# Kernel tuning notes

Measured on AMD Instinct MI355X. Metric: run time of the kernel, lower is better.

The kernel has to match this reference:

```python
import jax, jax.numpy as jnp
import numpy as np

CAPACITY_FACTOR = 1.2


def setup_inputs() -> dict:
    key = jax.random.key(0)
    k1, k2 = jax.random.split(key, 2)
    D, E = 1024, 64
    x = jax.random.normal(k1, (8, 4096, D), dtype=jnp.float32)
    # xavier-uniform-ish router weight, zero bias (as in __init__)
    limit = np.sqrt(6.0 / (D + E)).astype(np.float32)
    W = jax.random.uniform(k2, (E, D), dtype=jnp.float32, minval=-limit, maxval=limit)
    b = jnp.zeros((E,), dtype=jnp.float32)
    return {"x": x, "W": W, "b": b, "detach_inputs": 0}


def reference(x, W, b, detach_inputs):
    bsz, seqlen, D = x.shape
    E = W.shape[0]                      # num experts == max_steps
    N = bsz * seqlen                    # num tokens
    x_flat = x.reshape(N, D)
    if detach_inputs:
        x_flat = jax.lax.stop_gradient(x_flat)
    logits = x_flat @ W.T + b           # [N, E]

    # expert-choice capacity (static python ints)
    k = max(1, int(N / max(1, E) * CAPACITY_FACTOR))
    k = min(k, N)

    # per-expert top-k over tokens: [E, k]
    topk_vals, topk_idx = jax.lax.top_k(logits.T, k)
    cand_tok = topk_idx.reshape(-1)                       # [E*k] token ids
    cand_exp = jnp.repeat(jnp.arange(E, dtype=jnp.int32), k)  # [E*k]
    cand_val = topk_vals.reshape(-1)                      # [E*k]

    # scatter-amax: best candidate logit per token (torch scatter_reduce_ 'amax')
    best_val = jnp.full((N,), -jnp.inf, dtype=logits.dtype).at[cand_tok].max(cand_val)

    # candidates that achieve the per-token max; dedup -> one expert per token
    # (tie-break: smallest expert index, matching first-occurrence after sort)
    eq = cand_val == best_val[cand_tok]
    exp_cand = jnp.where(eq, cand_exp, E).astype(jnp.int32)
    token_exp = jnp.full((N,), E, dtype=jnp.int32).at[cand_tok].min(exp_cand)
    selected = token_exp < E                              # token was picked by some expert
    assigned_expert = jnp.where(selected, token_exp, -1)  # [N], -1 = unassigned

    # load-balance loss from per-expert counts (bincount of assigned experts)
    sel_f = selected.astype(logits.dtype)
    counts = jnp.zeros((E,), dtype=logits.dtype).at[jnp.where(selected, token_exp, 0)].add(sel_f)
    mean_load = counts.mean()
    load_balance_loss = ((counts - mean_load) ** 2).mean() / (mean_load + 1e-9)

    best_val_out = jnp.where(selected, best_val, jnp.zeros((), logits.dtype))
    return (best_val_out, assigned_expert, selected, load_balance_loss)
```

## Files before the change

### kernel.cpp

```cpp
#include <hip/hip_runtime.h>
#include <math.h>

typedef __attribute__((ext_vector_type(4))) double d4;

__device__ inline unsigned fkey(float f) {
  unsigned bits = __float_as_uint(f);
  return (bits & 0x80000000u) ? ~bits : (bits | 0x80000000u);
}

__global__ __launch_bounds__(1024, 8) void logits_fused_kernel(
    const float* __restrict__ x, const float* __restrict__ W,
    const float* __restrict__ bias, float* __restrict__ logits,
    float* __restrict__ logitsT, int N, int D) {
  __shared__ __attribute__((aligned(16))) double xbuf[2][64 * 33];
  __shared__ __attribute__((aligned(16))) double wbuf[2][64 * 33];
  __shared__ unsigned s_fl;

  const int tid = threadIdx.x;
  const int tok0 = blockIdx.x * 64;
  const int l = tid & 63;
  const int l15 = l & 15;
  const int lk = l >> 4;

  double* pA = &wbuf[0][0];
  double* pB = &wbuf[0][64];
  if (tid < 64) {
    pA[l15 * 4 + lk] = (double)(l15 * 4 + lk + 1);
    pB[lk * 16 + l15] = (double)(l15 * 7 + lk * 3 + 2);
  }
  __syncthreads();
  if (tid < 64) {
    double a = pA[l15 * 4 + lk];
    double b = pB[lk * 16 + l15];
    d4 pacc = (d4)0.0;
    pacc = __builtin_amdgcn_mfma_f64_16x16x4f64(a, b, pacc, 0, 0, 0);
    unsigned res = 4;
    for (int m = 3; m >= 0; --m) {
      bool ok = true;
#pragma unroll
      for (int i = 0; i < 4; ++i) {
        int tr_ = (m < 2) ? ((m == 0) ? 4 * lk + i : lk + 4 * i) : l15;
        int tc_ = (m < 2) ? l15 : ((m == 2) ? 4 * lk + i : lk + 4 * i);
        double ref = 0.0;
#pragma unroll
        for (int kk = 0; kk < 4; ++kk) ref += pA[tr_ * 4 + kk] * pB[kk * 16 + tc_];
        ok = ok && (pacc[i] == ref);
      }
      if (__all(ok)) res = (unsigned)m;
    }
    if (l == 0) s_fl = res;
  }
  __syncthreads();
  const unsigned fl = s_fl;
  __syncthreads();

  if (fl < 4u) {
    const int w = tid >> 6;
    const int rb = (w & 3) * 16;
    const int cb = (w >> 2) * 16;

    d4 acc = (d4)0.0;

    const int srow = (tid & 511) >> 3;
    const int sc = tid & 7;
    const bool isx = (tid < 512);
    const float* gsrc = isx ? (x + (size_t)(tok0 + srow) * D + sc * 4)
                            : (W + (size_t)srow * D + sc * 4);
    const int ldoff = srow * 33 + sc * 4;

    const int nch = D >> 5;
    const int xa0 = (rb + l15) * 33 + lk;
    const int ba0 = (cb + l15) * 33 + lk;

    float4 rg = *(const float4*)gsrc;
    {
      double* ld = (isx ? &xbuf[0][0] : &wbuf[0][0]) + ldoff;
      ld[0] = (double)rg.x; ld[1] = (double)rg.y;
      ld[2] = (double)rg.z; ld[3] = (double)rg.w;
    }
    if (nch > 1) rg = *(const float4*)(gsrc + 32);
    __syncthreads();

    for (int c = 0; c < nch; ++c) {
      const int cbuf = c & 1;
      const int nb = cbuf ^ 1;
      if (c + 1 < nch) {
        double* ld = (isx ? &xbuf[nb][0] : &wbuf[nb][0]) + ldoff;
        ld[0] = (double)rg.x; ld[1] = (double)rg.y;
        ld[2] = (double)rg.z; ld[3] = (double)rg.w;
        if (c + 2 < nch) rg = *(const float4*)(gsrc + (c + 2) * 32);
      }
      const double* xr = &xbuf[cbuf][0];
      const double* wr = &wbuf[cbuf][0];
#pragma unroll
      for (int s = 0; s < 8; ++s) {
        double a = xr[xa0 + 4 * s];
        double b = wr[ba0 + 4 * s];
        acc = __builtin_amdgcn_mfma_f64_16x16x4f64(a, b, acc, 0, 0, 0);
      }
      __syncthreads();
    }

    float* ls = (float*)&xbuf[0][0];
#pragma unroll
    for (int i = 0; i < 4; ++i) {
      int tr_, tc_;
      if (fl < 2u) { tc_ = l15; tr_ = (fl == 0u) ? 4 * lk + i : lk + 4 * i; }
      else         { tr_ = l15; tc_ = (fl == 2u) ? 4 * lk + i : lk + 4 * i; }
      int col = cb + tc_;
      ls[(rb + tr_) * 68 + col] = (float)(acc[i] + (double)bias[col]);
    }
    __syncthreads();
    {
      int row = tid >> 4, c4 = tid & 15;
      float4 v = {ls[row * 68 + c4 * 4 + 0], ls[row * 68 + c4 * 4 + 1],
                  ls[row * 68 + c4 * 4 + 2], ls[row * 68 + c4 * 4 + 3]};
      *(float4*)(logits + (size_t)(tok0 + row) * 64 + c4 * 4) = v;
    }
    {
      int e = tid >> 4, t4 = tid & 15;
      float4 v = {ls[(t4 * 4 + 0) * 68 + e], ls[(t4 * 4 + 1) * 68 + e],
                  ls[(t4 * 4 + 2) * 68 + e], ls[(t4 * 4 + 3) * 68 + e]};
      *(float4*)(logitsT + (size_t)e * N + tok0 + t4 * 4) = v;
    }
  } else {
    for (int o = tid; o < 64 * 64; o += 1024) {
      int row = o >> 6, col = o & 63;
      const float* xp = x + (size_t)(tok0 + row) * D;
      const float* wp = W + (size_t)col * D;
      double s = 0.0;
      for (int kk = 0; kk < D; ++kk)
        s = fma((double)xp[kk], (double)wp[kk], s);
      float v = (float)(s + (double)bias[col]);
      logits[(size_t)(tok0 + row) * 64 + col] = v;
      logitsT[(size_t)col * N + tok0 + row] = v;
    }
  }
}

template <int KPT4>
__global__ __launch_bounds__(1024) void select_kernel(
    const float* __restrict__ logitsT, unsigned* __restrict__ ukeys,
    int N, int k) {
  __shared__ unsigned long long part[16];
  __shared__ unsigned s_cur;
  const int e = blockIdx.x;
  const int tid = threadIdx.x;
  const int wid = tid >> 6;
  const int lane = tid & 63;

  const float4* src = (const float4*)(logitsT + (size_t)e * N);
  unsigned key[KPT4 > 0 ? KPT4 * 4 : 4];
  if (KPT4 > 0) {
#pragma unroll
    for (int i = 0; i < (KPT4 > 0 ? KPT4 : 1); ++i) {
      float4 v = src[tid + i * 1024];
      key[i * 4 + 0] = fkey(v.x);
      key[i * 4 + 1] = fkey(v.y);
      key[i * 4 + 2] = fkey(v.z);
      key[i * 4 + 3] = fkey(v.w);
    }
  }

  unsigned cur = 0;
  for (int s = 30; s >= 0; s -= 2) {
    unsigned c1 = cur | (1u << s);
    unsigned c2 = cur | (2u << s);
    unsigned c3 = cur | (3u << s);
    unsigned n1 = 0, n2 = 0, n3 = 0;
    if (KPT4 > 0) {
#pragma unroll
      for (int i = 0; i < (KPT4 > 0 ? KPT4 * 4 : 1); ++i) {
        unsigned u = key[i];
        n1 += (u >= c1) ? 1u : 0u;
        n2 += (u >= c2) ? 1u : 0u;
        n3 += (u >= c3) ? 1u : 0u;
      }
    } else {
      for (int i = tid; i < (N >> 2); i += 1024) {
        float4 v = src[i];
        unsigned u0 = fkey(v.x), u1 = fkey(v.y), u2 = fkey(v.z), u3 = fkey(v.w);
        n1 += (u0 >= c1) + (u1 >= c1) + (u2 >= c1) + (u3 >= c1);
        n2 += (u0 >= c2) + (u1 >= c2) + (u2 >= c2) + (u3 >= c2);
        n3 += (u0 >= c3) + (u1 >= c3) + (u2 >= c3) + (u3 >= c3);
      }
    }
    unsigned long long pk = (unsigned long long)n1 |
                            ((unsigned long long)n2 << 21) |
                            ((unsigned long long)n3 << 42);
#pragma unroll
    for (int off = 32; off; off >>= 1) pk += __shfl_xor(pk, off);
    if (lane == 0) part[wid] = pk;
    __syncthreads();
    if (tid == 0) {
      unsigned long long t = 0;
#pragma unroll
      for (int w = 0; w < 16; ++w) t += part[w];
      unsigned m1 = (unsigned)(t & 0x1FFFFFu);
      unsigned m2 = (unsigned)((t >> 21) & 0x1FFFFFu);
      unsigned m3 = (unsigned)(t >> 42);
      unsigned kk = (unsigned)k;
      unsigned nxt = cur;
      if (m3 >= kk) nxt = c3;
      else if (m2 >= kk) nxt = c2;
      else if (m1 >= kk) nxt = c1;
      s_cur = nxt;
    }
    __syncthreads();
    cur = s_cur;
  }
  if (tid == 0) ukeys[e] = cur;
}

__global__ __launch_bounds__(256) void assign_kernel(
    const float* __restrict__ logits, const unsigned* __restrict__ ukeys,
    float* __restrict__ out, int N) {
  const int lane = threadIdx.x & 63;
  const int token = blockIdx.x * 4 + (threadIdx.x >> 6);

  float v = logits[(size_t)token * 64 + lane];
  unsigned u = fkey(v);
  bool cand = (u >= ukeys[lane]);
  float cv = cand ? v : -INFINITY;
  float m = cv;
#pragma unroll
  for (int off = 32; off; off >>= 1) m = fmaxf(m, __shfl_xor(m, off));
  unsigned long long mask = __ballot(cand && (v == m));
  bool sel = (mask != 0ull);
  int minexp = sel ? (__ffsll((long long)mask) - 1) : -1;

  if (lane == 0) {
    out[token] = sel ? m : 0.0f;
    out[N + token] = (float)minexp;
    out[2 * N + token] = sel ? 1.0f : 0.0f;
  }
}

__global__ __launch_bounds__(1024) void count_loss_kernel(
    const float* __restrict__ assigned, float* __restrict__ out, int N) {
  __shared__ unsigned hist[16][64];
  const int tid = threadIdx.x;
  const int wid = tid >> 6;
  hist[wid][tid & 63] = 0u;
  __syncthreads();
  const float4* src = (const float4*)assigned;
  for (int i = tid; i < (N >> 2); i += 1024) {
    float4 v = src[i];
    int e0 = (int)v.x, e1 = (int)v.y, e2 = (int)v.z, e3 = (int)v.w;
    if (e0 >= 0) atomicAdd(&hist[wid][e0], 1u);
    if (e1 >= 0) atomicAdd(&hist[wid][e1], 1u);
    if (e2 >= 0) atomicAdd(&hist[wid][e2], 1u);
    if (e3 >= 0) atomicAdd(&hist[wid][e3], 1u);
  }
  __syncthreads();
  if (tid < 64) {
    unsigned c = 0;
#pragma unroll
    for (int w = 0; w < 16; ++w) c += hist[w][tid];
    double cd = (double)c;
    double s = cd;
#pragma unroll
    for (int off = 32; off; off >>= 1) s += __shfl_xor(s, off);
    double mean = s / 64.0;
    double d = cd - mean;
    d = d * d;
#pragma unroll
    for (int off = 32; off; off >>= 1) d += __shfl_xor(d, off);
    if (tid == 0) out[3 * (size_t)N] = (float)((d / 64.0) / (mean + 1e-9));
  }
}

extern "C" void kernel_launch(void* const* d_in, const int* in_sizes, int n_in,
                              void* d_out, int out_size, void* d_ws, size_t ws_size,
                              hipStream_t stream) {
  const float* x = (const float*)d_in[0];
  const float* W = (const float*)d_in[1];
  const float* b = (const float*)d_in[2];

  const int E = in_sizes[2];
  const int D = in_sizes[1] / E;
  const int N = in_sizes[0] / D;

  int k = (int)((double)N / (double)(E > 1 ? E : 1) * 1.2);
  if (k < 1) k = 1;
  if (k > N) k = N;

  const size_t NE = (size_t)N * E;
  float* out = (float*)d_out;

  float* logits = (float*)d_ws;
  float* logitsT = logits + NE;
  unsigned* ukeys = (unsigned*)(logitsT + NE);

  logits_fused_kernel<<<N / 64, 1024, 0, stream>>>(x, W, b, logits, logitsT,
                                                   N, D);
  if (N == 32768)
    select_kernel<8><<<64, 1024, 0, stream>>>(logitsT, ukeys, N, k);
  else
    select_kernel<0><<<64, 1024, 0, stream>>>(logitsT, ukeys, N, k);
  assign_kernel<<<N / 4, 256, 0, stream>>>(logits, ukeys, out, N);
  count_loss_kernel<<<1, 1024, 0, stream>>>(out + N, out, N);
}
```

Measured before the change: 125.9 us.

## Replace 2-bit radix threshold search with 8-bit histogram radix select

The per-expert k-th largest key search changes from 16 rounds of 2-bit counting (three threshold counts per round, block reductions and two syncs each) to 4 rounds of 8-bit radix selection. Each round builds per-wave shared-memory histograms with atomics, then one wave runs a suffix scan over 256 bins to pick the digit and the remaining rank. This cuts the number of passes over the register-resident keys and block barriers, in exchange for LDS atomic contention, which may be heavy in early rounds when many keys share a bin.

Result: faster. 110.5 us (median of 2 runs) (-12.2%).

```diff
diff --git a/kernel.cpp b/kernel.cpp
--- a/kernel.cpp
+++ b/kernel.cpp
@@ -142,12 +142,11 @@
 __global__ __launch_bounds__(1024) void select_kernel(
     const float* __restrict__ logitsT, unsigned* __restrict__ ukeys,
     int N, int k) {
-  __shared__ unsigned long long part[16];
-  __shared__ unsigned s_cur;
+  __shared__ unsigned hist[16][256];
+  __shared__ unsigned s_prefix, s_rem;
   const int e = blockIdx.x;
   const int tid = threadIdx.x;
   const int wid = tid >> 6;
-  const int lane = tid & 63;
 
   const float4* src = (const float4*)(logitsT + (size_t)e * N);
   unsigned key[KPT4 > 0 ? KPT4 * 4 : 4];
@@ -161,55 +160,64 @@
       key[i * 4 + 3] = fkey(v.w);
     }
   }
-
-  unsigned cur = 0;
-  for (int s = 30; s >= 0; s -= 2) {
-    unsigned c1 = cur | (1u << s);
-    unsigned c2 = cur | (2u << s);
-    unsigned c3 = cur | (3u << s);
-    unsigned n1 = 0, n2 = 0, n3 = 0;
+  if (tid == 0) { s_prefix = 0u; s_rem = (unsigned)k; }
+
+  for (int r = 0; r < 4; ++r) {
+    const int shift = 24 - 8 * r;
+    const unsigned maskhi = (r == 0) ? 0u : (0xFFFFFFFFu << (shift + 8));
+#pragma unroll
+    for (int z = 0; z < 4; ++z) ((unsigned*)hist)[z * 1024 + tid] = 0u;
+    __syncthreads();
+    const unsigned prefix = s_prefix;
     if (KPT4 > 0) {
 #pragma unroll
       for (int i = 0; i < (KPT4 > 0 ? KPT4 * 4 : 1); ++i) {
         unsigned u = key[i];
-        n1 += (u >= c1) ? 1u : 0u;
-        n2 += (u >= c2) ? 1u : 0u;
-        n3 += (u >= c3) ? 1u : 0u;
+        if ((u & maskhi) == prefix)
+          atomicAdd(&hist[wid][(u >> shift) & 255u], 1u);
       }
     } else {
       for (int i = tid; i < (N >> 2); i += 1024) {
         float4 v = src[i];
         unsigned u0 = fkey(v.x), u1 = fkey(v.y), u2 = fkey(v.z), u3 = fkey(v.w);
-        n1 += (u0 >= c1) + (u1 >= c1) + (u2 >= c1) + (u3 >= c1);
-        n2 += (u0 >= c2) + (u1 >= c2) + (u2 >= c2) + (u3 >= c2);
-        n3 += (u0 >= c3) + (u1 >= c3) + (u2 >= c3) + (u3 >= c3);
-      }
-    }
-    unsigned long long pk = (unsigned long long)n1 |
-                            ((unsigned long long)n2 << 21) |
-                            ((unsigned long long)n3 << 42);
-#pragma unroll
-    for (int off = 32; off; off >>= 1) pk += __shfl_xor(pk, off);
-    if (lane == 0) part[wid] = pk;
-    __syncthreads();
-    if (tid == 0) {
-      unsigned long long t = 0;
-#pragma unroll
-      for (int w = 0; w < 16; ++w) t += part[w];
-      unsigned m1 = (unsigned)(t & 0x1FFFFFu);
-      unsigned m2 = (unsigned)((t >> 21) & 0x1FFFFFu);
-      unsigned m3 = (unsigned)(t >> 42);
-      unsigned kk = (unsigned)k;
-      unsigned nxt = cur;
-      if (m3 >= kk) nxt = c3;
-      else if (m2 >= kk) nxt = c2;
-      else if (m1 >= kk) nxt = c1;
-      s_cur = nxt;
-    }
-    __syncthreads();
-    cur = s_cur;
-  }
-  if (tid == 0) ukeys[e] = cur;
+        if ((u0 & maskhi) == prefix) atomicAdd(&hist[wid][(u0 >> shift) & 255u], 1u);
+        if ((u1 & maskhi) == prefix) atomicAdd(&hist[wid][(u1 >> shift) & 255u], 1u);
+        if ((u2 & maskhi) == prefix) atomicAdd(&hist[wid][(u2 >> shift) & 255u], 1u);
+        if ((u3 & maskhi) == prefix) atomicAdd(&hist[wid][(u3 >> shift) & 255u], 1u);
+      }
+    }
+    __syncthreads();
+    if (tid < 64) {
+      unsigned rem = s_rem;
+      unsigned h0 = 0, h1 = 0, h2 = 0, h3 = 0;
+#pragma unroll
+      for (int w = 0; w < 16; ++w) {
+        h0 += hist[w][tid * 4 + 0];
+        h1 += hist[w][tid * 4 + 1];
+        h2 += hist[w][tid * 4 + 2];
+        h3 += hist[w][tid * 4 + 3];
+      }
+      unsigned c3 = h3, c2 = c3 + h2, c1 = c2 + h1, c0 = c1 + h0;
+      unsigned cum = c0;
+#pragma unroll
+      for (int off = 1; off < 64; off <<= 1) {
+        unsigned v = __shfl_down(cum, off);
+        if (tid + off < 64) cum += v;
+      }
+      unsigned above = cum - c0;
+      if (above < rem && rem <= cum) {
+        int j; unsigned abv;
+        if (above + c3 >= rem)      { j = 3; abv = above; }
+        else if (above + c2 >= rem) { j = 2; abv = above + c3; }
+        else if (above + c1 >= rem) { j = 1; abv = above + c2; }
+        else                        { j = 0; abv = above + c1; }
+        s_rem = rem - abv;
+        s_prefix = prefix | ((unsigned)(tid * 4 + j) << shift);
+      }
+    }
+    __syncthreads();
+  }
+  if (tid == 0) ukeys[e] = s_prefix;
 }
 
 __global__ __launch_bounds__(256) void assign_kernel(
```
